# Kernel optimization log

Hardware: AMD Instinct MI355X
Metric: run time of the kernel (lower is better)

## Reference

```python
import jax, jax.numpy as jnp
import numpy as np

T, D, S, Q, K = 768, 24, 576, 32, 128   # tokens, dense atoms/token, subsets, queries/subset, keys/subset
CA, CP, CT, H, DH = 128, 16, 384, 4, 32  # per-atom ch, pair ch, per-token ch, heads, head dim


def _conv_feat(idx, arr):
    # atom_layout.convert with layout_axes=(-3,-2): flatten first two axes, gather, keep channels
    return arr.reshape(-1, arr.shape[-1])[idx]


def _conv_flat(idx, arr):
    # atom_layout.convert with layout_axes=(-2,-1): flatten all layout axes, gather
    return arr.reshape(-1)[idx]


def setup_inputs() -> dict:
    key = jax.random.key(0)
    ks = iter(jax.random.split(key, 64))

    def nrm(shape, scale=0.05):
        return jax.random.normal(next(ks), shape, dtype=jnp.float32) * scale

    inp = {}
    inp["ref_positions"] = nrm((T, D, 3), 1.0)
    inp["ref_mask"] = jnp.ones((T, D), jnp.float32)
    inp["ref_charge"] = nrm((T, D), 1.0)
    inp["atom_mask"] = jnp.ones((T, D), jnp.float32)
    inp["ref_element"] = jax.random.randint(next(ks), (T, D), 0, 128)
    inp["ref_atom_name_chars"] = jax.random.randint(next(ks), (T, D, 4), 0, 64)
    inp["ref_space_uid"] = jax.random.randint(next(ks), (T, D), 0, T)
    inp["t2q_idx"] = jax.random.randint(next(ks), (S, Q), 0, T * D)
    inp["q2k_idx"] = jax.random.randint(next(ks), (S, K), 0, S * Q)
    inp["q2t_idx"] = jax.random.randint(next(ks), (T, D), 0, S * Q)
    # learned weights (stored (in, out); y = x @ W, equivalent to torch Linear with W.T)
    inp["w_ref_pos"] = nrm((3, CA))
    inp["w_ref_mask"] = nrm((1, CA))
    inp["w_ref_element"] = nrm((128, CA))
    inp["w_ref_charge"] = nrm((1, CA))
    inp["w_ref_atom_name"] = nrm((256, CA))
    inp["w_s2p_row1"] = nrm((CA, CP))
    inp["w_s2p_col1"] = nrm((CA, CP))
    inp["w_pair_off1"] = nrm((3, CP))
    inp["w_pair_dist1"] = nrm((1, CP))
    inp["w_pair_valid"] = nrm((1, CP))
    inp["w_mlp1"] = nrm((CP, CP))
    inp["w_mlp2"] = nrm((CP, CP))
    inp["w_mlp3"] = nrm((CP, CP))
    inp["wq"] = nrm((CA, H * DH))
    inp["wk"] = nrm((CA, H * DH))
    inp["wv"] = nrm((CA, H * DH))
    inp["wb"] = nrm((CP, H))
    inp["wo"] = nrm((H * DH, CA))
    inp["w_proj"] = nrm((CA, CT))
    return inp


def reference(ref_positions, ref_mask, ref_charge, atom_mask,
              ref_element, ref_atom_name_chars, ref_space_uid,
              t2q_idx, q2k_idx, q2t_idx,
              w_ref_pos, w_ref_mask, w_ref_element, w_ref_charge, w_ref_atom_name,
              w_s2p_row1, w_s2p_col1, w_pair_off1, w_pair_dist1, w_pair_valid,
              w_mlp1, w_mlp2, w_mlp3, wq, wk, wv, wb, wo, w_proj):
    # ---- per-atom conditioning ----
    act = ref_positions @ w_ref_pos                                   # (T,D,CA)
    act += ref_mask[..., None] @ w_ref_mask
    act += jax.nn.one_hot(ref_element, 128, dtype=jnp.float32) @ w_ref_element
    act += jnp.arcsinh(ref_charge)[..., None] @ w_ref_charge
    name_1hot = jax.nn.one_hot(ref_atom_name_chars, 64, dtype=jnp.float32).reshape(T, D, 256)
    act += name_1hot @ w_ref_atom_name
    act *= ref_mask[..., None]

    # ---- layout conversions (gathers) ----
    queries_single_cond = _conv_feat(t2q_idx, act)                    # (S,Q,CA)
    queries_mask = _conv_flat(t2q_idx, atom_mask)                     # (S,Q)
    queries_act = queries_single_cond
    keys_single_cond = _conv_feat(q2k_idx, queries_single_cond)       # (S,K,CA)
    keys_mask = _conv_flat(q2k_idx, queries_mask)                     # (S,K)

    # ---- pair conditioning: broadcast row+col, offsets, inv-sq-dist, validity ----
    row1 = jax.nn.relu(queries_single_cond) @ w_s2p_row1              # (S,Q,CP)
    col1 = jax.nn.relu(keys_single_cond) @ w_s2p_col1                 # (S,K,CP)
    pair = row1[:, :, None, :] + col1[:, None, :, :]                  # (S,Q,K,CP)

    queries_ref_pos = _conv_feat(t2q_idx, ref_positions)              # (S,Q,3)
    queries_uid = _conv_flat(t2q_idx, ref_space_uid)                  # (S,Q)
    keys_ref_pos = _conv_feat(q2k_idx, queries_ref_pos)               # (S,K,3)
    keys_uid = _conv_flat(q2k_idx, ref_space_uid)                     # (S,K)

    valid = (queries_uid[:, :, None] == keys_uid[:, None, :])         # (S,Q,K)
    validf = valid[..., None].astype(jnp.float32)
    offsets = queries_ref_pos[:, :, None, :] - keys_ref_pos[:, None, :, :]  # (S,Q,K,3)
    pair += (offsets @ w_pair_off1) * validf
    sq_dists = jnp.sum(jnp.square(offsets), axis=-1)
    pair += ((1.0 / (1.0 + sq_dists))[..., None] @ w_pair_dist1) * validf
    pair += validf @ w_pair_valid

    p2 = jax.nn.relu(pair) @ w_mlp1
    p2 = jax.nn.relu(p2) @ w_mlp2
    pair += jax.nn.relu(p2) @ w_mlp3

    # ---- cross-attention (queries attend to keys, pair_cond as bias) ----
    keys_act = _conv_feat(q2k_idx, queries_act)                       # (S,K,CA)
    q = (queries_act @ wq).reshape(S, Q, H, DH)
    k = (keys_act @ wk).reshape(S, K, H, DH)
    v = (keys_act @ wv).reshape(S, K, H, DH)
    bias = pair @ wb                                                  # (S,Q,K,H)
    logits = jnp.einsum('sqhd,skhd->sqkh', q, k) / jnp.sqrt(jnp.float32(DH)) + bias
    logits = jnp.where(keys_mask[:, None, :, None] > 0, logits, jnp.float32(-1e9))
    attn = jax.nn.softmax(logits, axis=2)
    o = jnp.einsum('sqkh,skhd->sqhd', attn, v).reshape(S, Q, H * DH)
    queries_act = queries_act + o @ wo

    queries_act = queries_act * queries_mask[..., None]
    skip_connection = queries_act
    proj = queries_act @ w_proj                                       # (S,Q,CT)
    token_atoms_act = _conv_feat(q2t_idx, proj)                       # (T,D,CT)

    # mask_mean over dense atom axis
    num = jnp.sum(atom_mask[..., None] * jax.nn.relu(token_atoms_act), axis=-2)
    den = jnp.sum(atom_mask, axis=-1, keepdims=True) + 1e-10
    token_act = num / den                                             # (T,CT)

    return (token_act, skip_connection, queries_mask, queries_single_cond,
            keys_mask, keys_single_cond, pair)
```

## Files before the change

kernel.cpp:

```cpp
#include <hip/hip_runtime.h>

typedef unsigned short u16;
typedef unsigned int u32;
typedef short bf16x8 __attribute__((ext_vector_type(8)));
typedef float f32x16 __attribute__((ext_vector_type(16)));

#define T_ 768
#define D_ 24
#define S_ 576
#define Q_ 32
#define K_ 128
#define CA_ 128
#define CP_ 16
#define CT_ 384
#define H_ 4
#define DH_ 32
#define SQ_ (S_*Q_)
#define SK_ (S_*K_)

__device__ __forceinline__ float b2f(u16 u){ return __uint_as_float(((u32)u)<<16); }
__device__ __forceinline__ u16 f2b(float f){ u32 x=__float_as_uint(f); return (u16)((x + 0x7fffu + ((x>>16)&1u))>>16); }

__global__ __launch_bounds__(128) void n_qsc(
    const float* __restrict__ pos, const float* __restrict__ rmask, const float* __restrict__ charge,
    const float* __restrict__ amask, const int* __restrict__ elem, const int* __restrict__ chars,
    const int* __restrict__ uid, const int* __restrict__ t2q,
    const float* __restrict__ w_pos, const float* __restrict__ w_mask, const float* __restrict__ w_elem,
    const float* __restrict__ w_chg, const float* __restrict__ w_name,
    float* __restrict__ qrp, int* __restrict__ quid,
    float* __restrict__ out_qsc, float* __restrict__ out_qmask)
{
  int ch = threadIdx.x;
  #pragma unroll 1
  for (int sl = 0; sl < 8; ++sl){
    int slot = blockIdx.x*8 + sl;
    int a = t2q[slot];
    float p0 = pos[a*3+0], p1 = pos[a*3+1], p2 = pos[a*3+2];
    float m  = rmask[a];
    float cg = asinhf(charge[a]);
    int e  = elem[a];
    int c0 = chars[a*4+0], c1 = chars[a*4+1], c2 = chars[a*4+2], c3 = chars[a*4+3];
    float v = p0*w_pos[0*CA_+ch] + p1*w_pos[1*CA_+ch] + p2*w_pos[2*CA_+ch];
    v += m * w_mask[ch];
    v += w_elem[e*CA_+ch];
    v += cg * w_chg[ch];
    v += w_name[(0*64+c0)*CA_+ch] + w_name[(1*64+c1)*CA_+ch]
       + w_name[(2*64+c2)*CA_+ch] + w_name[(3*64+c3)*CA_+ch];
    v *= m;
    out_qsc[(size_t)slot*CA_+ch] = v;
    if (ch < 3) qrp[slot*3+ch] = pos[a*3+ch];
    if (ch == 0){
      out_qmask[slot] = amask[a];
      quid[slot] = uid[a];
    }
  }
}

__global__ __launch_bounds__(128) void n_keys(
    const float* __restrict__ qsc, const float* __restrict__ qmask, const int* __restrict__ q2k,
    float* __restrict__ out_ksc, float* __restrict__ out_kmask)
{
  int e = threadIdx.x & 31;
  int rr = threadIdx.x >> 5;
  #pragma unroll
  for (int it = 0; it < 4; ++it){
    int sk = blockIdx.x*16 + it*4 + rr;
    int j = q2k[sk];
    *(float4*)&out_ksc[(size_t)sk*CA_ + e*4] = *(const float4*)&qsc[(size_t)j*CA_ + e*4];
    if (e == 0) out_kmask[sk] = qmask[j];
  }
}

__global__ __launch_bounds__(128) void n_qkv(
    const float* __restrict__ X, const float* __restrict__ wq, const float* __restrict__ wk,
    const float* __restrict__ wv, float* __restrict__ Qp, float* __restrict__ Kp, float* __restrict__ Vp)
{
  int c = threadIdx.x;
  size_t r0 = (size_t)blockIdx.x * 16;
  float aq[16], ak[16], av[16];
  #pragma unroll
  for (int r = 0; r < 16; ++r){ aq[r] = 0.f; ak[r] = 0.f; av[r] = 0.f; }
  #pragma unroll 4
  for (int i = 0; i < CA_; ++i){
    float q = wq[i*CA_+c];
    float k = wk[i*CA_+c];
    float v = wv[i*CA_+c];
    #pragma unroll
    for (int r = 0; r < 16; ++r){
      float x = X[(r0+r)*CA_ + i];
      aq[r] += x * q;
      ak[r] += x * k;
      av[r] += x * v;
    }
  }
  #pragma unroll
  for (int r = 0; r < 16; ++r){
    Qp[(r0+r)*CA_+c] = aq[r] * 0.17677669529663687f;
    Kp[(r0+r)*CA_+c] = ak[r];
    Vp[(r0+r)*CA_+c] = av[r];
  }
}

__global__ __launch_bounds__(128) void n_proj16b(
    const float* __restrict__ X, const float* __restrict__ Wr, const float* __restrict__ Wc,
    float* __restrict__ Yr, float* __restrict__ Yc)
{
  int row = blockIdx.x*4 + (threadIdx.x >> 5);
  int c = threadIdx.x & 31;
  const float* W = (c < 16) ? Wr : Wc;
  float* Y = (c < 16) ? Yr : Yc;
  int cc = c & 15;
  float acc = 0.f;
  for (int i = 0; i < CA_; ++i)
    acc += fmaxf(X[(size_t)row*CA_+i], 0.f) * W[i*CP_+cc];
  Y[(size_t)row*CP_+cc] = acc;
}

__global__ __launch_bounds__(128) void n_pair(
    const int* __restrict__ q2k, const float* __restrict__ rowproj, const float* __restrict__ colproj,
    const float* __restrict__ qrp, const int* __restrict__ quid, const int* __restrict__ uid,
    const float* __restrict__ w1, const float* __restrict__ w2, const float* __restrict__ w3,
    const float* __restrict__ wpo, const float* __restrict__ wpd, const float* __restrict__ wpv,
    const float* __restrict__ wb,
    float* __restrict__ out_pair, u16* __restrict__ bias_ws)
{
  int tid = threadIdx.x;
  int w   = tid >> 6;
  int l   = tid & 63;
  int lo  = l & 31;
  int hi  = l >> 5;
  int ch0 = hi * 8;
  int s   = blockIdx.x >> 2;
  int qg  = blockIdx.x & 3;

  float wox[8], woy[8], woz[8], wdd[8], wvv[8];
  *(float4*)&wox[0] = *(const float4*)&wpo[ch0];      *(float4*)&wox[4] = *(const float4*)&wpo[ch0+4];
  *(float4*)&woy[0] = *(const float4*)&wpo[16+ch0];   *(float4*)&woy[4] = *(const float4*)&wpo[16+ch0+4];
  *(float4*)&woz[0] = *(const float4*)&wpo[32+ch0];   *(float4*)&woz[4] = *(const float4*)&wpo[32+ch0+4];
  *(float4*)&wdd[0] = *(const float4*)&wpd[ch0];      *(float4*)&wdd[4] = *(const float4*)&wpd[ch0+4];
  *(float4*)&wvv[0] = *(const float4*)&wpv[ch0];      *(float4*)&wvv[4] = *(const float4*)&wpv[ch0+4];

  bf16x8 A1, A2, A3;
  #pragma unroll
  for (int j = 0; j < 8; ++j){ A1[j] = 0; A2[j] = 0; A3[j] = 0; }
  if (lo < 16){
    #pragma unroll
    for (int j = 0; j < 8; ++j){
      A1[j] = (short)f2b(w1[(ch0+j)*16 + lo]);
      A2[j] = (short)f2b(w2[(ch0+j)*16 + lo]);
      A3[j] = (short)f2b(w3[(ch0+j)*16 + lo]);
    }
  }
  f32x16 Z;
  #pragma unroll
  for (int i = 0; i < 16; ++i) Z[i] = 0.f;

  #pragma unroll 1
  for (int q4 = 0; q4 < 4; ++q4){
    int q  = qg*8 + w*4 + q4;
    int sq = s*Q_ + q;
    float qx = qrp[sq*3+0], qy = qrp[sq*3+1], qz = qrp[sq*3+2];
    int   qu = quid[sq];
    float rp[8];
    *(float4*)&rp[0] = *(const float4*)&rowproj[(size_t)sq*CP_ + ch0];
    *(float4*)&rp[4] = *(const float4*)&rowproj[(size_t)sq*CP_ + ch0 + 4];

    #pragma unroll 1
    for (int kb = 0; kb < 4; ++kb){
      int k  = kb*32 + lo;
      int sk = s*K_ + k;
      int j  = q2k[sk];
      float kx = qrp[j*3+0], ky = qrp[j*3+1], kz = qrp[j*3+2];
      int   ku = uid[j];
      float cp[8];
      *(float4*)&cp[0] = *(const float4*)&colproj[(size_t)j*CP_ + ch0];
      *(float4*)&cp[4] = *(const float4*)&colproj[(size_t)j*CP_ + ch0 + 4];

      float ox = qx - kx, oy = qy - ky, oz = qz - kz;
      float vf = (qu == ku) ? 1.f : 0.f;
      float invd = vf / (1.f + ox*ox + oy*oy + oz*oz);

      float p[8];
      #pragma unroll
      for (int jj = 0; jj < 8; ++jj)
        p[jj] = rp[jj] + cp[jj]
              + vf*(ox*wox[jj] + oy*woy[jj] + oz*woz[jj])
              + invd*wdd[jj] + vf*wvv[jj];

      bf16x8 bfr;
      #pragma unroll
      for (int jj = 0; jj < 8; ++jj) bfr[jj] = (short)f2b(fmaxf(p[jj], 0.f));
      f32x16 d = __builtin_amdgcn_mfma_f32_32x32x16_bf16(A1, bfr, Z, 0, 0, 0);

      float t[8];
      #pragma unroll
      for (int r = 0; r < 8; ++r) t[r] = __shfl_xor(d[r], 32, 64);
      #pragma unroll
      for (int jj = 0; jj < 4; ++jj){
        float v0 = hi ? t[jj+4] : d[jj];
        float v1 = hi ? d[jj+4] : t[jj];
        bfr[jj]   = (short)f2b(fmaxf(v0, 0.f));
        bfr[jj+4] = (short)f2b(fmaxf(v1, 0.f));
      }
      d = __builtin_amdgcn_mfma_f32_32x32x16_bf16(A2, bfr, Z, 0, 0, 0);
      #pragma unroll
      for (int r = 0; r < 8; ++r) t[r] = __shfl_xor(d[r], 32, 64);
      #pragma unroll
      for (int jj = 0; jj < 4; ++jj){
        float v0 = hi ? t[jj+4] : d[jj];
        float v1 = hi ? d[jj+4] : t[jj];
        bfr[jj]   = (short)f2b(fmaxf(v0, 0.f));
        bfr[jj+4] = (short)f2b(fmaxf(v1, 0.f));
      }
      d = __builtin_amdgcn_mfma_f32_32x32x16_bf16(A3, bfr, Z, 0, 0, 0);
      #pragma unroll
      for (int r = 0; r < 8; ++r) t[r] = __shfl_xor(d[r], 32, 64);
      float pout[8];
      #pragma unroll
      for (int jj = 0; jj < 4; ++jj){
        pout[jj]   = p[jj]   + (hi ? t[jj+4] : d[jj]);
        pout[jj+4] = p[jj+4] + (hi ? d[jj+4] : t[jj]);
      }

      size_t ob = ((size_t)sq*K_ + k)*CP_ + ch0;
      *(float4*)&out_pair[ob]     = make_float4(pout[0], pout[1], pout[2], pout[3]);
      *(float4*)&out_pair[ob + 4] = make_float4(pout[4], pout[5], pout[6], pout[7]);

      float b0 = 0.f, b1 = 0.f, b2 = 0.f, b3 = 0.f;
      #pragma unroll
      for (int jj = 0; jj < 8; ++jj){
        float4 wv4 = *(const float4*)&wb[(ch0+jj)*4];
        float pj = pout[jj];
        b0 += pj*wv4.x; b1 += pj*wv4.y; b2 += pj*wv4.z; b3 += pj*wv4.w;
      }
      b0 += __shfl_xor(b0, 32, 64);
      b1 += __shfl_xor(b1, 32, 64);
      b2 += __shfl_xor(b2, 32, 64);
      b3 += __shfl_xor(b3, 32, 64);
      if (hi == 0){
        size_t bb = (((size_t)s*H_ + 0)*Q_ + q)*K_ + k;
        bias_ws[bb]             = f2b(b0);
        bias_ws[bb + Q_*K_]     = f2b(b1);
        bias_ws[bb + 2*Q_*K_]   = f2b(b2);
        bias_ws[bb + 3*Q_*K_]   = f2b(b3);
      }
    }
  }
}

__global__ __launch_bounds__(128) void n_attn(
    const float* __restrict__ Qp, const float* __restrict__ Kp, const float* __restrict__ Vp,
    const float* __restrict__ qmask, const u16* __restrict__ bias_ws, const int* __restrict__ q2k,
    float* __restrict__ O)
{
  __shared__ float Ks[128*36];
  __shared__ float Vs[128*36];
  __shared__ float msk[128];
  __shared__ float redm[64];
  __shared__ float reds[64];
  __shared__ float Osm[32*33];

  int b = blockIdx.x;
  int s = b >> 2, h = b & 3;
  int sq0 = s * Q_;
  int base = s * K_;
  int t = threadIdx.x;

  {
    int e = t & 7, rr = t >> 3;
    #pragma unroll
    for (int it = 0; it < 8; ++it){
      int row = it*16 + rr;
      int j = q2k[base + row];
      const float4* ksrc = (const float4*)&Kp[(size_t)j*CA_ + h*DH_];
      const float4* vsrc = (const float4*)&Vp[(size_t)j*CA_ + h*DH_];
      *(float4*)&Ks[row*36 + e*4] = ksrc[e];
      *(float4*)&Vs[row*36 + e*4] = vsrc[e];
    }
    int j0 = q2k[base + t];
    msk[t] = qmask[j0];
  }

  int q  = t & 31;
  int kr = t >> 5;
  float qreg[32];
  {
    const float4* qsrc = (const float4*)&Qp[(size_t)(sq0+q)*CA_ + h*DH_];
    #pragma unroll
    for (int d4 = 0; d4 < 8; ++d4){
      float4 v = qsrc[d4];
      qreg[d4*4+0] = v.x; qreg[d4*4+1] = v.y; qreg[d4*4+2] = v.z; qreg[d4*4+3] = v.w;
    }
  }

  u32 bw[16];
  {
    const uint4* bsrc = (const uint4*)&bias_ws[(((size_t)s*H_ + h)*Q_ + q)*K_ + kr*32];
    uint4 B;
    B = bsrc[0]; bw[0]=B.x;  bw[1]=B.y;  bw[2]=B.z;  bw[3]=B.w;
    B = bsrc[1]; bw[4]=B.x;  bw[5]=B.y;  bw[6]=B.z;  bw[7]=B.w;
    B = bsrc[2]; bw[8]=B.x;  bw[9]=B.y;  bw[10]=B.z; bw[11]=B.w;
    B = bsrc[3]; bw[12]=B.x; bw[13]=B.y; bw[14]=B.z; bw[15]=B.w;
  }
  __syncthreads();

  float p[32];
  #pragma unroll
  for (int kk = 0; kk < 32; ++kk){
    int k = kr*32 + kk;
    const float* kbase = &Ks[k*36];
    float acc = 0.f;
    #pragma unroll
    for (int d4 = 0; d4 < 8; ++d4){
      float4 kv = *(const float4*)(kbase + d4*4);
      acc += qreg[d4*4+0]*kv.x + qreg[d4*4+1]*kv.y + qreg[d4*4+2]*kv.z + qreg[d4*4+3]*kv.w;
    }
    float bz = b2f((u16)((bw[kk>>1] >> ((kk&1)*16)) & 0xffffu));
    p[kk] = (msk[k] > 0.f) ? (acc + bz) : -1e9f;
  }

  float m = p[0];
  #pragma unroll
  for (int kk = 1; kk < 32; ++kk) m = fmaxf(m, p[kk]);
  m = fmaxf(m, __shfl_xor(m, 32, 64));
  int wv = t >> 6;
  if ((t & 63) < 32) redm[wv*32 + q] = m;
  __syncthreads();
  float M = fmaxf(redm[q], redm[32 + q]);

  float sm = 0.f;
  #pragma unroll
  for (int kk = 0; kk < 32; ++kk){ p[kk] = __expf(p[kk] - M); sm += p[kk]; }
  sm += __shfl_xor(sm, 32, 64);
  if ((t & 63) < 32) reds[wv*32 + q] = sm;
  __syncthreads();
  float inv = 1.f / (reds[q] + reds[32 + q]);

  float acc[32];
  #pragma unroll
  for (int d = 0; d < 32; ++d) acc[d] = 0.f;
  #pragma unroll
  for (int kk = 0; kk < 32; ++kk){
    float w = p[kk];
    const float* vbase = &Vs[(kr*32 + kk)*36];
    #pragma unroll
    for (int d4 = 0; d4 < 8; ++d4){
      float4 vv = *(const float4*)(vbase + d4*4);
      acc[d4*4+0] += w*vv.x; acc[d4*4+1] += w*vv.y; acc[d4*4+2] += w*vv.z; acc[d4*4+3] += w*vv.w;
    }
  }
  #pragma unroll
  for (int d = 0; d < 32; ++d) acc[d] += __shfl_xor(acc[d], 32, 64);
  if (t < 32){
    #pragma unroll
    for (int d = 0; d < 32; ++d) Osm[q*33 + d] = acc[d];
  }
  __syncthreads();
  if (t >= 64 && t < 96){
    #pragma unroll
    for (int d = 0; d < 32; ++d) Osm[q*33 + d] = (Osm[q*33 + d] + acc[d]) * inv;
  }
  __syncthreads();

  #pragma unroll
  for (int it = 0; it < 2; ++it){
    int idx = it*128 + t;
    int qq = idx >> 3, e = idx & 7;
    float4 v = make_float4(Osm[qq*33 + e*4 + 0], Osm[qq*33 + e*4 + 1],
                           Osm[qq*33 + e*4 + 2], Osm[qq*33 + e*4 + 3]);
    *(float4*)&O[(size_t)(sq0+qq)*CA_ + h*DH_ + e*4] = v;
  }
}

__global__ __launch_bounds__(128) void n_qact(
    const float* __restrict__ qsc, const float* __restrict__ O, const float* __restrict__ qmask,
    const float* __restrict__ wo, float* __restrict__ out_skip)
{
  int c = threadIdx.x;
  size_t r0 = (size_t)blockIdx.x * 16;
  float acc[16];
  #pragma unroll
  for (int r = 0; r < 16; ++r) acc[r] = 0.f;
  #pragma unroll 4
  for (int i = 0; i < CA_; ++i){
    float w = wo[i*CA_+c];
    #pragma unroll
    for (int r = 0; r < 16; ++r) acc[r] += O[(r0+r)*CA_+i] * w;
  }
  #pragma unroll
  for (int r = 0; r < 16; ++r){
    float v = (qsc[(r0+r)*CA_+c] + acc[r]) * qmask[r0+r];
    out_skip[(r0+r)*CA_+c] = v;
  }
}

__global__ __launch_bounds__(384) void n_tok(
    const float* __restrict__ qact, const int* __restrict__ q2t, const float* __restrict__ amask,
    const float* __restrict__ wp, float* __restrict__ out_tok)
{
  int t = blockIdx.x, ct = threadIdx.x;
  int jd[D_];
  float mk[D_];
  #pragma unroll
  for (int d = 0; d < D_; ++d){
    jd[d] = q2t[t*D_ + d];
    mk[d] = amask[t*D_ + d];
  }
  float acc[D_];
  #pragma unroll
  for (int d = 0; d < D_; ++d) acc[d] = 0.f;
  #pragma unroll 4
  for (int i = 0; i < CA_; ++i){
    float w = wp[i*CT_ + ct];
    #pragma unroll
    for (int d = 0; d < D_; ++d) acc[d] += qact[(size_t)jd[d]*CA_ + i] * w;
  }
  float num = 0.f, den = 1e-10f;
  #pragma unroll
  for (int d = 0; d < D_; ++d){
    num += mk[d] * fmaxf(acc[d], 0.f);
    den += mk[d];
  }
  out_tok[(size_t)t*CT_ + ct] = num/den;
}

extern "C" void kernel_launch(void* const* d_in, const int* in_sizes, int n_in,
                              void* d_out, int out_size, void* d_ws, size_t ws_size,
                              hipStream_t stream) {
  (void)in_sizes; (void)n_in; (void)out_size; (void)ws_size;
  const float* ref_positions = (const float*)d_in[0];
  const float* ref_mask      = (const float*)d_in[1];
  const float* ref_charge    = (const float*)d_in[2];
  const float* atom_mask     = (const float*)d_in[3];
  const int*   ref_element   = (const int*)d_in[4];
  const int*   ref_chars     = (const int*)d_in[5];
  const int*   ref_uid       = (const int*)d_in[6];
  const int*   t2q           = (const int*)d_in[7];
  const int*   q2k           = (const int*)d_in[8];
  const int*   q2t           = (const int*)d_in[9];
  const float* w_ref_pos     = (const float*)d_in[10];
  const float* w_ref_mask    = (const float*)d_in[11];
  const float* w_ref_element = (const float*)d_in[12];
  const float* w_ref_charge  = (const float*)d_in[13];
  const float* w_ref_name    = (const float*)d_in[14];
  const float* w_s2p_row1    = (const float*)d_in[15];
  const float* w_s2p_col1    = (const float*)d_in[16];
  const float* w_pair_off1   = (const float*)d_in[17];
  const float* w_pair_dist1  = (const float*)d_in[18];
  const float* w_pair_valid  = (const float*)d_in[19];
  const float* w_mlp1        = (const float*)d_in[20];
  const float* w_mlp2        = (const float*)d_in[21];
  const float* w_mlp3        = (const float*)d_in[22];
  const float* wq            = (const float*)d_in[23];
  const float* wk            = (const float*)d_in[24];
  const float* wv            = (const float*)d_in[25];
  const float* wb            = (const float*)d_in[26];
  const float* wo            = (const float*)d_in[27];
  const float* w_proj        = (const float*)d_in[28];

  char* ws = (char*)d_ws;
  float* qrp     = (float*)(ws + 9732096);
  int*   quid    = (int*)  (ws + 9953280);
  float* rowproj = (float*)(ws + 11206656);
  float* colproj = (float*)(ws + 12386304);
  float* Qp      = (float*)(ws + 13565952);
  float* Kp      = (float*)(ws + 23003136);
  float* Vp      = (float*)(ws + 32440320);
  float* O       = (float*)(ws + 41877504);
  u16*   biasws  = (u16*)  (ws + 60751872);

  float* out = (float*)d_out;
  float* out_tok   = out + 0;
  float* out_skip  = out + 294912;
  float* out_qmask = out + 2654208;
  float* out_qsc   = out + 2672640;
  float* out_kmask = out + 5031936;
  float* out_ksc   = out + 5105664;
  float* out_pair  = out + 14542848;

  hipLaunchKernelGGL(n_qsc, dim3(SQ_/8), dim3(128), 0, stream,
      ref_positions, ref_mask, ref_charge, atom_mask, ref_element, ref_chars, ref_uid, t2q,
      w_ref_pos, w_ref_mask, w_ref_element, w_ref_charge, w_ref_name,
      qrp, quid, out_qsc, out_qmask);
  hipLaunchKernelGGL(n_keys, dim3(SK_/16), dim3(128), 0, stream,
      out_qsc, out_qmask, q2k, out_ksc, out_kmask);
  hipLaunchKernelGGL(n_qkv, dim3(SQ_/16), dim3(128), 0, stream,
      out_qsc, wq, wk, wv, Qp, Kp, Vp);
  hipLaunchKernelGGL(n_proj16b, dim3(SQ_/4), dim3(128), 0, stream,
      out_qsc, w_s2p_row1, w_s2p_col1, rowproj, colproj);
  hipLaunchKernelGGL(n_pair, dim3(S_*4), dim3(128), 0, stream,
      q2k, rowproj, colproj, qrp, quid, ref_uid,
      w_mlp1, w_mlp2, w_mlp3, w_pair_off1, w_pair_dist1, w_pair_valid, wb,
      out_pair, biasws);
  hipLaunchKernelGGL(n_attn, dim3(S_*H_), dim3(128), 0, stream,
      Qp, Kp, Vp, out_qmask, biasws, q2k, O);
  hipLaunchKernelGGL(n_qact, dim3(SQ_/16), dim3(128), 0, stream,
      out_qsc, O, out_qmask, wo, out_skip);
  hipLaunchKernelGGL(n_tok, dim3(T_), dim3(384), 0, stream,
      out_skip, q2t, atom_mask, w_proj, out_tok);
}
```

Before: 532.8 us.

## Rewrite attention kernel as single-wave bf16 MFMA with LDS-staged bias

Replaces the scalar-FMA fp32 attention kernel with a single-wavefront block that computes QK^T and PV using 32x32x16 bf16 MFMA instructions, converting Q, K, V and probabilities to bf16 in registers. The bias tile is expanded into LDS, and the key mask is read directly from the precomputed keys-mask output instead of gathering through q2k. This removes the LDS staging of K/V and the cross-wave reductions and syncthreads. In exchange it lowers precision of the logits and of the PV product to bf16, and V is gathered with scalar strided loads.

```diff
diff --git a/kernel.cpp b/kernel.cpp
--- a/kernel.cpp
+++ b/kernel.cpp
@@ -20,6 +20,12 @@
 
 __device__ __forceinline__ float b2f(u16 u){ return __uint_as_float(((u32)u)<<16); }
 __device__ __forceinline__ u16 f2b(float f){ u32 x=__float_as_uint(f); return (u16)((x + 0x7fffu + ((x>>16)&1u))>>16); }
+
+__device__ __forceinline__ void wave_fence(){
+  __builtin_amdgcn_sched_barrier(0);
+  __builtin_amdgcn_wave_barrier();
+  __builtin_amdgcn_sched_barrier(0);
+}
 
 __global__ __launch_bounds__(128) void n_qsc(
     const float* __restrict__ pos, const float* __restrict__ rmask, const float* __restrict__ charge,
@@ -248,127 +254,141 @@
   }
 }
 
-__global__ __launch_bounds__(128) void n_attn(
+__global__ __launch_bounds__(64) void n_attn(
     const float* __restrict__ Qp, const float* __restrict__ Kp, const float* __restrict__ Vp,
-    const float* __restrict__ qmask, const u16* __restrict__ bias_ws, const int* __restrict__ q2k,
+    const float* __restrict__ kmask, const u16* __restrict__ bias_ws, const int* __restrict__ q2k,
     float* __restrict__ O)
 {
-  __shared__ float Ks[128*36];
-  __shared__ float Vs[128*36];
-  __shared__ float msk[128];
-  __shared__ float redm[64];
-  __shared__ float reds[64];
-  __shared__ float Osm[32*33];
-
+  __shared__ float Ls[32*129];
+  __shared__ float msk[K_];
+  int t  = threadIdx.x;
+  int lo = t & 31, hi = t >> 5;
   int b = blockIdx.x;
   int s = b >> 2, h = b & 3;
-  int sq0 = s * Q_;
-  int base = s * K_;
-  int t = threadIdx.x;
+  int sq0 = s*Q_, base = s*K_;
+
+  msk[t]      = kmask[base + t];
+  msk[64 + t] = kmask[base + 64 + t];
 
   {
-    int e = t & 7, rr = t >> 3;
-    #pragma unroll
-    for (int it = 0; it < 8; ++it){
-      int row = it*16 + rr;
-      int j = q2k[base + row];
-      const float4* ksrc = (const float4*)&Kp[(size_t)j*CA_ + h*DH_];
-      const float4* vsrc = (const float4*)&Vp[(size_t)j*CA_ + h*DH_];
-      *(float4*)&Ks[row*36 + e*4] = ksrc[e];
-      *(float4*)&Vs[row*36 + e*4] = vsrc[e];
-    }
-    int j0 = q2k[base + t];
-    msk[t] = qmask[j0];
-  }
-
-  int q  = t & 31;
-  int kr = t >> 5;
-  float qreg[32];
+    const uint2* bsrc = (const uint2*)&bias_ws[(size_t)(s*H_ + h)*Q_*K_];
+    #pragma unroll
+    for (int i = 0; i < 16; ++i){
+      int idx = i*64 + t;
+      int q = idx >> 5, e = (idx & 31)*4;
+      uint2 v = bsrc[idx];
+      float* dst = &Ls[q*129 + e];
+      dst[0] = b2f((u16)(v.x & 0xffffu));
+      dst[1] = b2f((u16)(v.x >> 16));
+      dst[2] = b2f((u16)(v.y & 0xffffu));
+      dst[3] = b2f((u16)(v.y >> 16));
+    }
+  }
+
+  bf16x8 Bq1, Bq2;
   {
-    const float4* qsrc = (const float4*)&Qp[(size_t)(sq0+q)*CA_ + h*DH_];
-    #pragma unroll
-    for (int d4 = 0; d4 < 8; ++d4){
-      float4 v = qsrc[d4];
-      qreg[d4*4+0] = v.x; qreg[d4*4+1] = v.y; qreg[d4*4+2] = v.z; qreg[d4*4+3] = v.w;
-    }
-  }
-
-  u32 bw[16];
-  {
-    const uint4* bsrc = (const uint4*)&bias_ws[(((size_t)s*H_ + h)*Q_ + q)*K_ + kr*32];
-    uint4 B;
-    B = bsrc[0]; bw[0]=B.x;  bw[1]=B.y;  bw[2]=B.z;  bw[3]=B.w;
-    B = bsrc[1]; bw[4]=B.x;  bw[5]=B.y;  bw[6]=B.z;  bw[7]=B.w;
-    B = bsrc[2]; bw[8]=B.x;  bw[9]=B.y;  bw[10]=B.z; bw[11]=B.w;
-    B = bsrc[3]; bw[12]=B.x; bw[13]=B.y; bw[14]=B.z; bw[15]=B.w;
-  }
-  __syncthreads();
-
-  float p[32];
-  #pragma unroll
-  for (int kk = 0; kk < 32; ++kk){
-    int k = kr*32 + kk;
-    const float* kbase = &Ks[k*36];
-    float acc = 0.f;
-    #pragma unroll
-    for (int d4 = 0; d4 < 8; ++d4){
-      float4 kv = *(const float4*)(kbase + d4*4);
-      acc += qreg[d4*4+0]*kv.x + qreg[d4*4+1]*kv.y + qreg[d4*4+2]*kv.z + qreg[d4*4+3]*kv.w;
-    }
-    float bz = b2f((u16)((bw[kk>>1] >> ((kk&1)*16)) & 0xffffu));
-    p[kk] = (msk[k] > 0.f) ? (acc + bz) : -1e9f;
-  }
-
-  float m = p[0];
-  #pragma unroll
-  for (int kk = 1; kk < 32; ++kk) m = fmaxf(m, p[kk]);
-  m = fmaxf(m, __shfl_xor(m, 32, 64));
-  int wv = t >> 6;
-  if ((t & 63) < 32) redm[wv*32 + q] = m;
-  __syncthreads();
-  float M = fmaxf(redm[q], redm[32 + q]);
-
+    const float* qrow = &Qp[(size_t)(sq0+lo)*CA_ + h*DH_];
+    float4 x0 = *(const float4*)&qrow[hi*8];
+    float4 x1 = *(const float4*)&qrow[hi*8+4];
+    float4 x2 = *(const float4*)&qrow[16+hi*8];
+    float4 x3 = *(const float4*)&qrow[16+hi*8+4];
+    Bq1[0]=(short)f2b(x0.x); Bq1[1]=(short)f2b(x0.y); Bq1[2]=(short)f2b(x0.z); Bq1[3]=(short)f2b(x0.w);
+    Bq1[4]=(short)f2b(x1.x); Bq1[5]=(short)f2b(x1.y); Bq1[6]=(short)f2b(x1.z); Bq1[7]=(short)f2b(x1.w);
+    Bq2[0]=(short)f2b(x2.x); Bq2[1]=(short)f2b(x2.y); Bq2[2]=(short)f2b(x2.z); Bq2[3]=(short)f2b(x2.w);
+    Bq2[4]=(short)f2b(x3.x); Bq2[5]=(short)f2b(x3.y); Bq2[6]=(short)f2b(x3.z); Bq2[7]=(short)f2b(x3.w);
+  }
+
+  f32x16 Z;
+  #pragma unroll
+  for (int i = 0; i < 16; ++i) Z[i] = 0.f;
+
+  f32x16 Sar[4];
+  #pragma unroll
+  for (int n = 0; n < 4; ++n){
+    int jkn = q2k[base + 32*n + lo];
+    const float* krow = &Kp[(size_t)jkn*CA_ + h*DH_];
+    float4 x0 = *(const float4*)&krow[hi*8];
+    float4 x1 = *(const float4*)&krow[hi*8+4];
+    float4 x2 = *(const float4*)&krow[16+hi*8];
+    float4 x3 = *(const float4*)&krow[16+hi*8+4];
+    bf16x8 Ak1, Ak2;
+    Ak1[0]=(short)f2b(x0.x); Ak1[1]=(short)f2b(x0.y); Ak1[2]=(short)f2b(x0.z); Ak1[3]=(short)f2b(x0.w);
+    Ak1[4]=(short)f2b(x1.x); Ak1[5]=(short)f2b(x1.y); Ak1[6]=(short)f2b(x1.z); Ak1[7]=(short)f2b(x1.w);
+    Ak2[0]=(short)f2b(x2.x); Ak2[1]=(short)f2b(x2.y); Ak2[2]=(short)f2b(x2.z); Ak2[3]=(short)f2b(x2.w);
+    Ak2[4]=(short)f2b(x3.x); Ak2[5]=(short)f2b(x3.y); Ak2[6]=(short)f2b(x3.z); Ak2[7]=(short)f2b(x3.w);
+    f32x16 d = __builtin_amdgcn_mfma_f32_32x32x16_bf16(Ak1, Bq1, Z, 0, 0, 0);
+    Sar[n]   = __builtin_amdgcn_mfma_f32_32x32x16_bf16(Ak2, Bq2, d, 0, 0, 0);
+  }
+
+  wave_fence();
+
+  float e_[4][16];
+  float mx = -1e30f;
+  #pragma unroll
+  for (int n = 0; n < 4; ++n){
+    #pragma unroll
+    for (int r = 0; r < 16; ++r){
+      int k = 32*n + (r&3) + 8*(r>>2) + 4*hi;
+      float lg = (msk[k] > 0.f) ? (Sar[n][r] + Ls[lo*129 + k]) : -1e9f;
+      e_[n][r] = lg;
+      mx = fmaxf(mx, lg);
+    }
+  }
+  mx = fmaxf(mx, __shfl_xor(mx, 32, 64));
   float sm = 0.f;
   #pragma unroll
-  for (int kk = 0; kk < 32; ++kk){ p[kk] = __expf(p[kk] - M); sm += p[kk]; }
+  for (int n = 0; n < 4; ++n){
+    #pragma unroll
+    for (int r = 0; r < 16; ++r){
+      float ee = __expf(e_[n][r] - mx);
+      e_[n][r] = ee;
+      sm += ee;
+    }
+  }
   sm += __shfl_xor(sm, 32, 64);
-  if ((t & 63) < 32) reds[wv*32 + q] = sm;
-  __syncthreads();
-  float inv = 1.f / (reds[q] + reds[32 + q]);
-
-  float acc[32];
-  #pragma unroll
-  for (int d = 0; d < 32; ++d) acc[d] = 0.f;
-  #pragma unroll
-  for (int kk = 0; kk < 32; ++kk){
-    float w = p[kk];
-    const float* vbase = &Vs[(kr*32 + kk)*36];
-    #pragma unroll
-    for (int d4 = 0; d4 < 8; ++d4){
-      float4 vv = *(const float4*)(vbase + d4*4);
-      acc[d4*4+0] += w*vv.x; acc[d4*4+1] += w*vv.y; acc[d4*4+2] += w*vv.z; acc[d4*4+3] += w*vv.w;
-    }
-  }
-  #pragma unroll
-  for (int d = 0; d < 32; ++d) acc[d] += __shfl_xor(acc[d], 32, 64);
-  if (t < 32){
-    #pragma unroll
-    for (int d = 0; d < 32; ++d) Osm[q*33 + d] = acc[d];
-  }
-  __syncthreads();
-  if (t >= 64 && t < 96){
-    #pragma unroll
-    for (int d = 0; d < 32; ++d) Osm[q*33 + d] = (Osm[q*33 + d] + acc[d]) * inv;
-  }
-  __syncthreads();
-
-  #pragma unroll
-  for (int it = 0; it < 2; ++it){
-    int idx = it*128 + t;
-    int qq = idx >> 3, e = idx & 7;
-    float4 v = make_float4(Osm[qq*33 + e*4 + 0], Osm[qq*33 + e*4 + 1],
-                           Osm[qq*33 + e*4 + 2], Osm[qq*33 + e*4 + 3]);
-    *(float4*)&O[(size_t)(sq0+qq)*CA_ + h*DH_ + e*4] = v;
+  float inv = 1.f / sm;
+
+  f32x16 Dpv = Z;
+  #pragma unroll
+  for (int mt = 0; mt < 8; ++mt){
+    bf16x8 Av;
+    #pragma unroll
+    for (int j = 0; j < 8; ++j){
+      int kk = 16*mt + hi*8 + j;
+      int jv = q2k[base + kk];
+      Av[j] = (short)f2b(Vp[(size_t)jv*CA_ + h*DH_ + lo]);
+    }
+    bf16x8 Bp;
+    int n  = mt >> 1;
+    int m1 = mt & 1;
+    #pragma unroll
+    for (int j = 0; j < 4; ++j){
+      int r0 = j + 8*m1;
+      int r1 = r0 + 4;
+      float o0 = e_[n][r0];
+      float o1 = e_[n][r1];
+      float x0 = __shfl_xor(o0, 32, 64);
+      float x1 = __shfl_xor(o1, 32, 64);
+      Bp[j]   = (short)f2b(hi ? x1 : o0);
+      Bp[j+4] = (short)f2b(hi ? o1 : x0);
+    }
+    Dpv = __builtin_amdgcn_mfma_f32_32x32x16_bf16(Av, Bp, Dpv, 0, 0, 0);
+  }
+
+  wave_fence();
+  #pragma unroll
+  for (int b2 = 0; b2 < 4; ++b2){
+    *(float4*)&Ls[lo*33 + 8*b2 + 4*hi] =
+      make_float4(Dpv[4*b2+0]*inv, Dpv[4*b2+1]*inv, Dpv[4*b2+2]*inv, Dpv[4*b2+3]*inv);
+  }
+  wave_fence();
+  #pragma unroll
+  for (int it = 0; it < 4; ++it){
+    int fid = it*64 + t;
+    int qq = fid >> 3, e4 = fid & 7;
+    float4 v = make_float4(Ls[qq*33 + e4*4 + 0], Ls[qq*33 + e4*4 + 1],
+                           Ls[qq*33 + e4*4 + 2], Ls[qq*33 + e4*4 + 3]);
+    *(float4*)&O[(size_t)(sq0+qq)*CA_ + h*DH_ + e4*4] = v;
   }
 }
 
@@ -492,8 +512,8 @@
       q2k, rowproj, colproj, qrp, quid, ref_uid,
       w_mlp1, w_mlp2, w_mlp3, w_pair_off1, w_pair_dist1, w_pair_valid, wb,
       out_pair, biasws);
-  hipLaunchKernelGGL(n_attn, dim3(S_*H_), dim3(128), 0, stream,
-      Qp, Kp, Vp, out_qmask, biasws, q2k, O);
+  hipLaunchKernelGGL(n_attn, dim3(S_*H_), dim3(64), 0, stream,
+      Qp, Kp, Vp, out_kmask, biasws, q2k, O);
   hipLaunchKernelGGL(n_qact, dim3(SQ_/16), dim3(128), 0, stream,
       out_qsc, O, out_qmask, wo, out_skip);
   hipLaunchKernelGGL(n_tok, dim3(T_), dim3(384), 0, stream,
```

After: 515.3 us. 3.3% less time.
